# Performance work log

Hardware: AMD Instinct MI355X
Metric: run time of the kernel (lower is better)

The kernel has to match this reference:

```python
import jax, jax.numpy as jnp
import numpy as np

N = 512          # num_atoms (sqrt of number of pairwise edges)
H = 512          # h_nf / in_edge_nf
T_STEPS = 100    # recon.total_time
K_RANK = 3       # coord_dims / low-rank k
POWER_STEPS = 10


def setup_inputs() -> dict:
    key = jax.random.key(0)
    ks = jax.random.split(key, 6)
    s = 1.0 / np.sqrt(H)
    return {
        "gnn_edge_out": jax.random.normal(ks[0], (N * N, H), jnp.float32),
        "W1": jax.random.normal(ks[1], (H, H), jnp.float32) * s,   # edge_mlp1 Linear
        "b1": jnp.zeros((H,), jnp.float32),
        "W2": jax.random.normal(ks[2], (H, 2), jnp.float32) * s,    # edge_mlp2 Linear(h_nf, edge_out_nf=2)
        "b2": jnp.zeros((2,), jnp.float32),
        "noise_x": jax.random.normal(ks[3], (N, K_RANK), jnp.float32),  # randn added to low-rank init
        "u_init": jax.random.normal(ks[4], (N, K_RANK), jnp.float32),   # power-iteration random starts
    }


def reference(gnn_edge_out, W1, b1, W2, b2, noise_x, u_init):
    # ---- DistWeightLayer ----
    h = jax.nn.relu(gnn_edge_out @ W1 + b1)          # edge_mlp1 (MLP, 1 layer)
    emb = jnp.sum(h)[None]                           # sum over dims (0,1), unsqueeze -> (1,)
    e = jax.nn.softplus(h @ W2 + b2)                 # (N*N, 2) softplus(edge_mlp2)
    D_init = e[:, 0].reshape(N, N) * (1.0 - jnp.eye(N, dtype=e.dtype))
    W = e[:, 1].reshape(N, N)

    # ---- dist_to_gram ----
    D = D_init
    D_row = jnp.mean(D, axis=0)                      # (N,)
    D_col = jnp.mean(D, axis=1, keepdims=True)       # (N,1)
    D_mean = jnp.mean(D)
    B = -0.5 * (D - D_row - D_col + D_mean)

    # ---- low_rank_approx_power (k=3, deflation) ----
    A_lr = B
    us = []
    for i in range(K_RANK):
        u = u_init[:, i:i + 1]                       # (N,1)
        for _ in range(POWER_STEPS):
            u = u / jnp.maximum(jnp.linalg.norm(u), 1e-3)  # F.normalize eps=0.001
            u = A_lr @ u
        eig_sq = jnp.sum(u * u)
        u = u * (eig_sq + 0.01) ** 0.25              # u / pow(eig_sq+0.01, -0.25)
        us.append(u)
        A_lr = A_lr - u @ u.T
    X = jnp.concatenate(us, axis=1) + noise_x        # (N,3)

    # ---- 100-step distance-geometry descent (step_func) ----
    def U_fn(Xc):
        diff = Xc[:, None, :] - Xc[None, :, :]       # (N,N,3)
        Dx = jnp.sqrt(jnp.sum(diff * diff, axis=-1) + 0.01)  # tsg_eps
        return jnp.sum(W * jnp.square(D_init - Dx))

    def step(Xc, t):
        g = jax.grad(U_fn)(Xc)
        dX = -0.1 * g                                # tsg_eps1
        speed = jnp.sqrt(jnp.sum(dX * dX, axis=-1, keepdims=True) + 0.001)  # tsg_eps2
        alpha_t = 0.1 + (5.0 - 0.1) * (T_STEPS - t) / T_STEPS
        scale = alpha_t * jnp.tanh(speed / alpha_t) / speed
        return Xc + dX * scale, None

    X_pred, _ = jax.lax.scan(step, X, jnp.arange(T_STEPS, dtype=X.dtype))
    return (D_init, W, emb, X_pred)
```

## Files before the change

kernel.cpp:

```cpp
#include <hip/hip_runtime.h>
#include <hip/hip_bf16.h>
#include <math.h>

#define NN 512
#define ROWS (NN * NN)
#define HH 512

#define NB 16
#define NT 512
#define RPB 32

#define WS_EMB   0
#define WS_COLP  4096
#define WS_U0    (WS_COLP + 32*512)
#define WS_U1    (WS_U0 + 512)
#define WS_X0    (WS_U1 + 512)
#define WS_X1    (WS_X0 + 2048)
#define WS_W1F   (WS_X1 + 2048)
#define WS_BAR   (WS_W1F + 131072)

typedef __attribute__((ext_vector_type(8))) short bf16x8;
typedef __attribute__((ext_vector_type(4))) float f32x4;

#define AGENT __HIP_MEMORY_SCOPE_AGENT

__device__ __forceinline__ short f2bf(float f) {
    union { float f; unsigned u; } v; v.f = f;
    unsigned r = v.u + 0x7fffu + ((v.u >> 16) & 1u);
    return (short)(r >> 16);
}

__device__ __forceinline__ unsigned pack_bf2(float lo, float hi) {
    return __builtin_amdgcn_perm(__float_as_uint(hi), __float_as_uint(lo),
                                 0x07060302u);
}

__device__ __forceinline__ float softplus_f(float x) {
    return fmaxf(x, 0.0f) + log1pf(expf(-fabsf(x)));
}

__device__ __forceinline__ unsigned long long pk64(float a, float b) {
    return ((unsigned long long)__float_as_uint(b) << 32) |
           (unsigned long long)__float_as_uint(a);
}

__global__ void w1f_prep(const float* __restrict__ W1, short* __restrict__ W1F)
{
    const int c = blockIdx.x * 256 + threadIdx.x;
    const int lane = c & 63;
    const int g = c >> 6;
    const int colg = g & 31;
    const int kc = g >> 5;
    const int col = colg * 16 + (lane & 15);
    const int kb = kc * 32 + (lane >> 4) * 8;
    bf16x8 w;
    #pragma unroll
    for (int j = 0; j < 8; j++)
        w[j] = f2bf(W1[(size_t)(kb + j) * HH + col]);
    *(bf16x8*)(W1F + (size_t)c * 8) = w;
}

__global__ __launch_bounds__(512, 4) void fused_mlp(
    const float* __restrict__ A, const short* __restrict__ W1F,
    const float* __restrict__ b1, const float* __restrict__ W2,
    const float* __restrict__ b2, float* __restrict__ outD,
    float* __restrict__ outW, float* __restrict__ embpart)
{
    __shared__ short As[2][64 * 40];
    __shared__ float sp0[8][64], sp1[8][64];
    __shared__ float semb[8];

    const int tid = threadIdx.x;
    const int lane = tid & 63;
    const int wc = tid >> 6;
    const int l15 = lane & 15;
    const int l4 = lane >> 4;
    const int row0 = blockIdx.x * 64;

    f32x4 acc[4][4];
    #pragma unroll
    for (int m = 0; m < 4; m++)
        #pragma unroll
        for (int n = 0; n < 4; n++) {
            f32x4 z = {0.0f, 0.0f, 0.0f, 0.0f};
            acc[m][n] = z;
        }

    const int sr = tid >> 3;
    const int sk4 = (tid & 7) * 4;
    const float* agp = A + (size_t)(row0 + sr) * HH + sk4;

    const short* bfp = W1F + ((size_t)(wc * 4) * 64 + lane) * 8;

    {
        float4 a0 = *(const float4*)agp;
        uint2 w = {pack_bf2(a0.x, a0.y), pack_bf2(a0.z, a0.w)};
        *(uint2*)&As[0][sr * 40 + sk4] = w;
    }
    bf16x8 bfr[4];
    #pragma unroll
    for (int n = 0; n < 4; n++)
        bfr[n] = *(const bf16x8*)(bfp + n * 512);
    __syncthreads();

    int cur = 0;
    #pragma unroll 1
    for (int s = 0; s < 16; s++) {
        const int k0 = s * 32;
        bf16x8 bfrN[4];
        if (s < 15) {
            #pragma unroll
            for (int n = 0; n < 4; n++)
                bfrN[n] = *(const bf16x8*)(bfp + (s + 1) * 16384 + n * 512);
        }
        float4 pv;
        if (s < 15) pv = *(const float4*)(agp + k0 + 32);
        bf16x8 af[4];
        #pragma unroll
        for (int m = 0; m < 4; m++)
            af[m] = *(const bf16x8*)&As[cur][(m * 16 + l15) * 40 + l4 * 8];
        #pragma unroll
        for (int m = 0; m < 4; m++)
            #pragma unroll
            for (int n = 0; n < 4; n++)
                acc[m][n] = __builtin_amdgcn_mfma_f32_16x16x32_bf16(
                    af[m], bfr[n], acc[m][n], 0, 0, 0);
        if (s < 15) {
            uint2 w = {pack_bf2(pv.x, pv.y), pack_bf2(pv.z, pv.w)};
            *(uint2*)&As[cur ^ 1][sr * 40 + sk4] = w;
            #pragma unroll
            for (int n = 0; n < 4; n++) bfr[n] = bfrN[n];
        }
        __syncthreads();
        cur ^= 1;
    }

    float b1c[4], w20[4], w21[4];
    #pragma unroll
    for (int n = 0; n < 4; n++) {
        int col = wc * 64 + n * 16 + l15;
        b1c[n] = b1[col];
        w20[n] = W2[col * 2 + 0];
        w21[n] = W2[col * 2 + 1];
    }
    float embl = 0.0f;
    #pragma unroll
    for (int m = 0; m < 4; m++) {
        #pragma unroll
        for (int j = 0; j < 4; j++) {
            float s0 = 0.0f, s1 = 0.0f;
            #pragma unroll
            for (int n = 0; n < 4; n++) {
                float h = fmaxf(acc[m][n][j] + b1c[n], 0.0f);
                s0 = fmaf(h, w20[n], s0);
                s1 = fmaf(h, w21[n], s1);
                embl += h;
            }
            #pragma unroll
            for (int st = 1; st < 16; st <<= 1) {
                s0 += __shfl_xor(s0, st);
                s1 += __shfl_xor(s1, st);
            }
            if (l15 == 0) {
                int row = m * 16 + l4 * 4 + j;
                sp0[wc][row] = s0;
                sp1[wc][row] = s1;
            }
        }
    }
    #pragma unroll
    for (int st = 1; st < 64; st <<= 1) embl += __shfl_xor(embl, st);
    if (lane == 0) semb[wc] = embl;
    __syncthreads();
    if (tid < 64) {
        int gr = row0 + tid;
        float p0 = b2[0], p1 = b2[1];
        #pragma unroll
        for (int w = 0; w < 8; w++) { p0 += sp0[w][tid]; p1 += sp1[w][tid]; }
        int di = gr >> 9, dj = gr & 511;
        outD[gr] = (di == dj) ? 0.0f : softplus_f(p0);
        outW[gr] = softplus_f(p1);
    }
    if (tid == 0) {
        float e = 0.0f;
        #pragma unroll
        for (int w = 0; w < 8; w++) e += semb[w];
        embpart[blockIdx.x] = e;
    }
}

__device__ __forceinline__ void gbar(int* cnt, int target)
{
    __syncthreads();
    if (threadIdx.x == 0)
        __hip_atomic_fetch_add(cnt, 1, __ATOMIC_RELAXED, AGENT);
    if (threadIdx.x < 64) {
        while (__hip_atomic_load(cnt, __ATOMIC_RELAXED, AGENT) < target)
            __builtin_amdgcn_s_sleep(1);
    }
    __syncthreads();
}

__device__ __forceinline__ void block_sum5(float* v, float (*red)[8], int tid) {
    #pragma unroll
    for (int s = 1; s < 64; s <<= 1)
        #pragma unroll
        for (int q = 0; q < 5; q++) v[q] += __shfl_xor(v[q], s);
    if ((tid & 63) == 0)
        #pragma unroll
        for (int q = 0; q < 5; q++) red[q][tid >> 6] = v[q];
    __syncthreads();
    #pragma unroll
    for (int q = 0; q < 5; q++) {
        float r = 0.0f;
        #pragma unroll
        for (int i = 0; i < 8; i++) r += red[q][i];
        v[q] = r;
    }
    __syncthreads();
}

__device__ __forceinline__ float block_sum1(float v, float (*red)[8], int tid) {
    #pragma unroll
    for (int s = 1; s < 64; s <<= 1) v += __shfl_xor(v, s);
    if ((tid & 63) == 0) red[0][tid >> 6] = v;
    __syncthreads();
    float r = 0.0f;
    #pragma unroll
    for (int i = 0; i < 8; i++) r += red[0][i];
    __syncthreads();
    return r;
}

__global__ __launch_bounds__(512, 1) void coop_post(
    const float* __restrict__ Dg, const float* __restrict__ Wg,
    const float* __restrict__ noise, const float* __restrict__ uinit,
    float* __restrict__ outE, float* __restrict__ outX,
    float* __restrict__ ws)
{
    __shared__ float Dl[RPB][516];
    __shared__ float S1[RPB][516];
    __shared__ float Xl[512][4];
    __shared__ float ul[512];
    __shared__ float upl[3][512];
    __shared__ float cm[512];
    __shared__ float rm[RPB];
    __shared__ float red5[5][8];

    const int tid = threadIdx.x;
    const int bid = blockIdx.x;
    const int r0 = bid * RPB;

    float* embpart = ws + WS_EMB;
    float* colpart = ws + WS_COLP;
    float* ubuf0   = ws + WS_U0;
    float* ubuf1   = ws + WS_U1;
    float* Xg0     = ws + WS_X0;
    float* Xg1     = ws + WS_X1;
    int* cnt       = (int*)(ws + WS_BAR);
    int bg = 0;

    for (int idx = tid; idx < RPB * 512; idx += NT) {
        int r = idx >> 9, c = idx & 511;
        Dl[r][c] = Dg[(size_t)(r0 + r) * NN + c];
    }
    __syncthreads();
    const int mr = tid >> 4;
    const int ml = tid & 15;
    {
        float s = 0.0f;
        for (int j = ml; j < 512; j += 16) s += Dl[mr][j];
        #pragma unroll
        for (int st = 1; st < 16; st <<= 1) s += __shfl_xor(s, st);
        if (ml == 0) rm[mr] = s * (1.0f / 512.0f);
    }
    {
        float s = 0.0f;
        #pragma unroll
        for (int r = 0; r < RPB; r++) s += Dl[r][tid];
        __hip_atomic_store(&colpart[bid * 512 + tid], s, __ATOMIC_RELAXED, AGENT);
    }
    gbar(cnt, NB * ++bg);

    {
        float s = 0.0f;
        #pragma unroll
        for (int p = 0; p < NB; p++)
            s += __hip_atomic_load(&colpart[p * 512 + tid], __ATOMIC_RELAXED, AGENT);
        cm[tid] = s * (1.0f / 512.0f);
    }
    if (bid == 0) {
        float s = 0.0f;
        for (int i = tid; i < ROWS / 64; i += NT) s += embpart[i];
        s = block_sum1(s, red5, tid);
        if (tid == 0) outE[0] = s;
    }
    __syncthreads();
    float Dmean = block_sum1(cm[tid], red5, tid) * (1.0f / 512.0f);

    int cur = 0;
    #pragma unroll 1
    for (int rank = 0; rank < 3; rank++) {
        #pragma unroll 1
        for (int step = 0; step < 10; step++) {
            if (step == 0) {
                ul[tid] = uinit[tid * 3 + rank];
            } else {
                const float* ub = cur ? ubuf1 : ubuf0;
                ul[tid] = __hip_atomic_load(&ub[tid], __ATOMIC_RELAXED, AGENT);
            }
            __syncthreads();
            float u = ul[tid];
            float v[5];
            v[0] = u * u;
            v[1] = u;
            v[2] = cm[tid] * u;
            v[3] = (rank > 0) ? upl[0][tid] * u : 0.0f;
            v[4] = (rank > 1) ? upl[1][tid] * u : 0.0f;
            block_sum5(v, red5, tid);
            float inv = 1.0f / fmaxf(sqrtf(v[0]), 0.001f);
            float S = v[1] * inv, dr = v[2] * inv;
            float d0s = v[3] * inv, d1s = v[4] * inv;
            float a = 0.0f;
            for (int j = ml; j < 512; j += 16) a = fmaf(Dl[mr][j], ul[j], a);
            #pragma unroll
            for (int st = 1; st < 16; st <<= 1) a += __shfl_xor(a, st);
            if (ml == 0) {
                float bvv = -0.5f * (a * inv - dr - rm[mr] * S + Dmean * S);
                if (rank > 0) bvv -= d0s * upl[0][r0 + mr];
                if (rank > 1) bvv -= d1s * upl[1][r0 + mr];
                float* ubn = cur ? ubuf0 : ubuf1;
                __hip_atomic_store(&ubn[r0 + mr], bvv, __ATOMIC_RELAXED, AGENT);
            }
            gbar(cnt, NB * ++bg);
            cur ^= 1;
        }
        {
            const float* ub = cur ? ubuf1 : ubuf0;
            float u = __hip_atomic_load(&ub[tid], __ATOMIC_RELAXED, AGENT);
            float eig2 = block_sum1(u * u, red5, tid);
            float scl = sqrtf(sqrtf(eig2 + 0.01f));
            upl[rank][tid] = u * scl;
            Xl[tid][rank] = fmaf(u, scl, noise[tid * 3 + rank]);
            if (rank == 0) Xl[tid][3] = 0.0f;
            __syncthreads();
        }
    }

    for (int idx = tid; idx < RPB * 512; idx += NT) {
        int r = idx >> 9, j = idx & 511;
        int gr = r0 + r;
        float wr = Wg[(size_t)gr * NN + j];
        float wc = Wg[(size_t)j * NN + gr];
        float dc = Dg[(size_t)j * NN + gr];
        float d  = Dl[r][j];
        S1[r][j] = wr + wc;
        Dl[r][j] = fmaf(wr, d, wc * dc);
    }
    __syncthreads();

    unsigned long long* X064 = (unsigned long long*)Xg0;
    unsigned long long* X164 = (unsigned long long*)Xg1;
    int par = 0;
    #pragma unroll 1
    for (int t = 0; t < 100; t++) {
        float xr0 = Xl[r0 + mr][0], xr1 = Xl[r0 + mr][1], xr2 = Xl[r0 + mr][2];
        float g0 = 0, g1 = 0, g2 = 0;
        for (int j = ml; j < 512; j += 16) {
            float dx0 = xr0 - Xl[j][0];
            float dx1 = xr1 - Xl[j][1];
            float dx2 = xr2 - Xl[j][2];
            float d2 = fmaf(dx0, dx0, fmaf(dx1, dx1, fmaf(dx2, dx2, 0.01f)));
            float ri = rsqrtf(d2);
            float coef = fmaf(Dl[mr][j], ri, -S1[mr][j]);
            g0 = fmaf(coef, dx0, g0);
            g1 = fmaf(coef, dx1, g1);
            g2 = fmaf(coef, dx2, g2);
        }
        #pragma unroll
        for (int st = 1; st < 16; st <<= 1) {
            g0 += __shfl_xor(g0, st);
            g1 += __shfl_xor(g1, st);
            g2 += __shfl_xor(g2, st);
        }
        if (ml == 0) {
            float dX0 = 0.2f * g0, dX1 = 0.2f * g1, dX2 = 0.2f * g2;
            float sp = sqrtf(fmaf(dX0, dX0, fmaf(dX1, dX1, fmaf(dX2, dX2, 0.001f))));
            float alpha = 0.1f + 4.9f * (float)(100 - t) * 0.01f;
            float scal = alpha * tanhf(sp / alpha) / sp;
            float n0 = fmaf(dX0, scal, xr0);
            float n1 = fmaf(dX1, scal, xr1);
            float n2 = fmaf(dX2, scal, xr2);
            int gr = r0 + mr;
            if (t == 99) {
                outX[gr * 3 + 0] = n0;
                outX[gr * 3 + 1] = n1;
                outX[gr * 3 + 2] = n2;
            } else {
                unsigned long long* Xd64 = par ? X164 : X064;
                __hip_atomic_store(&Xd64[gr * 2], pk64(n0, n1),
                                   __ATOMIC_RELAXED, AGENT);
                __hip_atomic_store(&Xd64[gr * 2 + 1], pk64(n2, 0.0f),
                                   __ATOMIC_RELAXED, AGENT);
            }
        }
        if (t == 99) break;
        gbar(cnt, NB * ++bg);
        {
            const unsigned long long* Xs64 = par ? X164 : X064;
            unsigned long long lo =
                __hip_atomic_load(&Xs64[tid * 2], __ATOMIC_RELAXED, AGENT);
            unsigned long long hi =
                __hip_atomic_load(&Xs64[tid * 2 + 1], __ATOMIC_RELAXED, AGENT);
            Xl[tid][0] = __uint_as_float((unsigned)lo);
            Xl[tid][1] = __uint_as_float((unsigned)(lo >> 32));
            Xl[tid][2] = __uint_as_float((unsigned)hi);
            Xl[tid][3] = 0.0f;
        }
        __syncthreads();
        par ^= 1;
    }
}

extern "C" void kernel_launch(void* const* d_in, const int* in_sizes, int n_in,
                              void* d_out, int out_size, void* d_ws, size_t ws_size,
                              hipStream_t stream)
{
    const float* A     = (const float*)d_in[0];
    const float* W1    = (const float*)d_in[1];
    const float* b1    = (const float*)d_in[2];
    const float* W2    = (const float*)d_in[3];
    const float* b2    = (const float*)d_in[4];
    const float* noise = (const float*)d_in[5];
    const float* uinit = (const float*)d_in[6];

    float* out  = (float*)d_out;
    float* outD = out;
    float* outW = out + ROWS;
    float* outE = out + 2 * ROWS;
    float* outX = out + 2 * ROWS + 1;
    float* ws   = (float*)d_ws;
    short* W1F  = (short*)(ws + WS_W1F);

    (void)hipMemsetAsync((char*)d_ws + (size_t)WS_BAR * sizeof(float), 0,
                         512 * sizeof(int), stream);

    hipLaunchKernelGGL(w1f_prep, dim3(128), dim3(256), 0, stream, W1, W1F);

    hipLaunchKernelGGL(fused_mlp, dim3(ROWS / 64), dim3(512), 0, stream,
                       A, W1F, b1, W2, b2, outD, outW, ws + WS_EMB);

    const float* Dg  = outD;
    const float* Wgc = outW;
    void* args[] = { (void*)&Dg, (void*)&Wgc, (void*)&noise, (void*)&uinit,
                     (void*)&outE, (void*)&outX, (void*)&ws };
    (void)hipLaunchCooperativeKernel((const void*)coop_post, dim3(NB), dim3(NT),
                                     args, 0, stream);
}
```

Measured before the change: 865.3 us.

## Replace global counter barriers with generation-tagged per-value flags in cooperative kernel

Removes the atomic-counter grid barrier and instead packs each exchanged float with a generation tag in a 64-bit word, so consumers spin until the value carrying the expected generation appears. The aim is to drop the full barrier round trip (fetch-add plus spin plus two syncthreads) from each of the roughly 130 iterations of the power-iteration and descent loops, letting blocks proceed as soon as their data is ready. In exchange every thread polls its own slots, which adds more memory traffic and relies on double buffering plus generation numbers being enough to avoid overwriting slots before they are read. The memset now clears the larger exchange region.

```diff
diff --git a/kernel.cpp b/kernel.cpp
--- a/kernel.cpp
+++ b/kernel.cpp
@@ -11,13 +11,8 @@
 #define RPB 32
 
 #define WS_EMB   0
-#define WS_COLP  4096
-#define WS_U0    (WS_COLP + 32*512)
-#define WS_U1    (WS_U0 + 512)
-#define WS_X0    (WS_U1 + 512)
-#define WS_X1    (WS_X0 + 2048)
-#define WS_W1F   (WS_X1 + 2048)
-#define WS_BAR   (WS_W1F + 131072)
+#define WS_W1F   4096
+#define WS_XCH   (WS_W1F + 131072)
 
 typedef __attribute__((ext_vector_type(8))) short bf16x8;
 typedef __attribute__((ext_vector_type(4))) float f32x4;
@@ -39,9 +34,19 @@
     return fmaxf(x, 0.0f) + log1pf(expf(-fabsf(x)));
 }
 
-__device__ __forceinline__ unsigned long long pk64(float a, float b) {
-    return ((unsigned long long)__float_as_uint(b) << 32) |
-           (unsigned long long)__float_as_uint(a);
+__device__ __forceinline__ void pub64(unsigned long long* p, float val, int gen) {
+    unsigned long long v = ((unsigned long long)(unsigned)gen << 32) |
+                           (unsigned long long)__float_as_uint(val);
+    __hip_atomic_store(p, v, __ATOMIC_RELAXED, AGENT);
+}
+__device__ __forceinline__ float poll64(const unsigned long long* p, int gen) {
+    unsigned long long v;
+    for (;;) {
+        v = __hip_atomic_load(p, __ATOMIC_RELAXED, AGENT);
+        if ((int)(v >> 32) == gen) break;
+        __builtin_amdgcn_s_sleep(1);
+    }
+    return __uint_as_float((unsigned)v);
 }
 
 __global__ void w1f_prep(const float* __restrict__ W1, short* __restrict__ W1F)
@@ -89,7 +94,6 @@
     const int sr = tid >> 3;
     const int sk4 = (tid & 7) * 4;
     const float* agp = A + (size_t)(row0 + sr) * HH + sk4;
-
     const short* bfp = W1F + ((size_t)(wc * 4) * 64 + lane) * 8;
 
     {
@@ -187,18 +191,6 @@
         for (int w = 0; w < 8; w++) e += semb[w];
         embpart[blockIdx.x] = e;
     }
-}
-
-__device__ __forceinline__ void gbar(int* cnt, int target)
-{
-    __syncthreads();
-    if (threadIdx.x == 0)
-        __hip_atomic_fetch_add(cnt, 1, __ATOMIC_RELAXED, AGENT);
-    if (threadIdx.x < 64) {
-        while (__hip_atomic_load(cnt, __ATOMIC_RELAXED, AGENT) < target)
-            __builtin_amdgcn_s_sleep(1);
-    }
-    __syncthreads();
 }
 
 __device__ __forceinline__ void block_sum5(float* v, float (*red)[8], int tid) {
@@ -252,13 +244,10 @@
     const int r0 = bid * RPB;
 
     float* embpart = ws + WS_EMB;
-    float* colpart = ws + WS_COLP;
-    float* ubuf0   = ws + WS_U0;
-    float* ubuf1   = ws + WS_U1;
-    float* Xg0     = ws + WS_X0;
-    float* Xg1     = ws + WS_X1;
-    int* cnt       = (int*)(ws + WS_BAR);
-    int bg = 0;
+    unsigned long long* xch = (unsigned long long*)(ws + WS_XCH);
+    unsigned long long* colp  = xch;
+    unsigned long long* uslot = xch + 8192;
+    unsigned long long* xslot = xch + 9216;
 
     for (int idx = tid; idx < RPB * 512; idx += NT) {
         int r = idx >> 9, c = idx & 511;
@@ -278,15 +267,14 @@
         float s = 0.0f;
         #pragma unroll
         for (int r = 0; r < RPB; r++) s += Dl[r][tid];
-        __hip_atomic_store(&colpart[bid * 512 + tid], s, __ATOMIC_RELAXED, AGENT);
-    }
-    gbar(cnt, NB * ++bg);
+        pub64(&colp[bid * 512 + tid], s, 1);
+    }
 
     {
         float s = 0.0f;
-        #pragma unroll
+        #pragma unroll 1
         for (int p = 0; p < NB; p++)
-            s += __hip_atomic_load(&colpart[p * 512 + tid], __ATOMIC_RELAXED, AGENT);
+            s += poll64(&colp[p * 512 + tid], 1);
         cm[tid] = s * (1.0f / 512.0f);
     }
     if (bid == 0) {
@@ -298,16 +286,15 @@
     __syncthreads();
     float Dmean = block_sum1(cm[tid], red5, tid) * (1.0f / 512.0f);
 
-    int cur = 0;
     #pragma unroll 1
     for (int rank = 0; rank < 3; rank++) {
         #pragma unroll 1
         for (int step = 0; step < 10; step++) {
+            const int s3 = rank * 10 + step;
             if (step == 0) {
                 ul[tid] = uinit[tid * 3 + rank];
             } else {
-                const float* ub = cur ? ubuf1 : ubuf0;
-                ul[tid] = __hip_atomic_load(&ub[tid], __ATOMIC_RELAXED, AGENT);
+                ul[tid] = poll64(&uslot[((s3 - 1) & 1) * 512 + tid], s3);
             }
             __syncthreads();
             float u = ul[tid];
@@ -329,15 +316,12 @@
                 float bvv = -0.5f * (a * inv - dr - rm[mr] * S + Dmean * S);
                 if (rank > 0) bvv -= d0s * upl[0][r0 + mr];
                 if (rank > 1) bvv -= d1s * upl[1][r0 + mr];
-                float* ubn = cur ? ubuf0 : ubuf1;
-                __hip_atomic_store(&ubn[r0 + mr], bvv, __ATOMIC_RELAXED, AGENT);
-            }
-            gbar(cnt, NB * ++bg);
-            cur ^= 1;
+                pub64(&uslot[(s3 & 1) * 512 + r0 + mr], bvv, s3 + 1);
+            }
         }
         {
-            const float* ub = cur ? ubuf1 : ubuf0;
-            float u = __hip_atomic_load(&ub[tid], __ATOMIC_RELAXED, AGENT);
+            const int s3l = rank * 10 + 9;
+            float u = poll64(&uslot[(s3l & 1) * 512 + tid], s3l + 1);
             float eig2 = block_sum1(u * u, red5, tid);
             float scl = sqrtf(sqrtf(eig2 + 0.01f));
             upl[rank][tid] = u * scl;
@@ -359,11 +343,25 @@
     }
     __syncthreads();
 
-    unsigned long long* X064 = (unsigned long long*)Xg0;
-    unsigned long long* X164 = (unsigned long long*)Xg1;
-    int par = 0;
     #pragma unroll 1
     for (int t = 0; t < 100; t++) {
+        if (t > 0) {
+            const unsigned long long* xs = xslot + ((t - 1) & 1) * 1536 + tid * 3;
+            unsigned long long w0, w1, w2;
+            for (;;) {
+                w0 = __hip_atomic_load(&xs[0], __ATOMIC_RELAXED, AGENT);
+                w1 = __hip_atomic_load(&xs[1], __ATOMIC_RELAXED, AGENT);
+                w2 = __hip_atomic_load(&xs[2], __ATOMIC_RELAXED, AGENT);
+                if ((int)(w0 >> 32) == t && (int)(w1 >> 32) == t &&
+                    (int)(w2 >> 32) == t) break;
+                __builtin_amdgcn_s_sleep(1);
+            }
+            Xl[tid][0] = __uint_as_float((unsigned)w0);
+            Xl[tid][1] = __uint_as_float((unsigned)w1);
+            Xl[tid][2] = __uint_as_float((unsigned)w2);
+            Xl[tid][3] = 0.0f;
+            __syncthreads();
+        }
         float xr0 = Xl[r0 + mr][0], xr1 = Xl[r0 + mr][1], xr2 = Xl[r0 + mr][2];
         float g0 = 0, g1 = 0, g2 = 0;
         for (int j = ml; j < 512; j += 16) {
@@ -397,28 +395,12 @@
                 outX[gr * 3 + 1] = n1;
                 outX[gr * 3 + 2] = n2;
             } else {
-                unsigned long long* Xd64 = par ? X164 : X064;
-                __hip_atomic_store(&Xd64[gr * 2], pk64(n0, n1),
-                                   __ATOMIC_RELAXED, AGENT);
-                __hip_atomic_store(&Xd64[gr * 2 + 1], pk64(n2, 0.0f),
-                                   __ATOMIC_RELAXED, AGENT);
-            }
-        }
-        if (t == 99) break;
-        gbar(cnt, NB * ++bg);
-        {
-            const unsigned long long* Xs64 = par ? X164 : X064;
-            unsigned long long lo =
-                __hip_atomic_load(&Xs64[tid * 2], __ATOMIC_RELAXED, AGENT);
-            unsigned long long hi =
-                __hip_atomic_load(&Xs64[tid * 2 + 1], __ATOMIC_RELAXED, AGENT);
-            Xl[tid][0] = __uint_as_float((unsigned)lo);
-            Xl[tid][1] = __uint_as_float((unsigned)(lo >> 32));
-            Xl[tid][2] = __uint_as_float((unsigned)hi);
-            Xl[tid][3] = 0.0f;
-        }
-        __syncthreads();
-        par ^= 1;
+                unsigned long long* xd = xslot + (t & 1) * 1536 + gr * 3;
+                pub64(&xd[0], n0, t + 1);
+                pub64(&xd[1], n1, t + 1);
+                pub64(&xd[2], n2, t + 1);
+            }
+        }
     }
 }
 
@@ -442,8 +424,8 @@
     float* ws   = (float*)d_ws;
     short* W1F  = (short*)(ws + WS_W1F);
 
-    (void)hipMemsetAsync((char*)d_ws + (size_t)WS_BAR * sizeof(float), 0,
-                         512 * sizeof(int), stream);
+    (void)hipMemsetAsync((char*)d_ws + (size_t)WS_XCH * sizeof(float), 0,
+                         12288 * sizeof(unsigned long long), stream);
 
     hipLaunchKernelGGL(w1f_prep, dim3(128), dim3(256), 0, stream, W1, W1F);
 
```

New measurement: 901.8 us. +4.2%, slower.
